# Performance work log

Measured on AMD Instinct MI355X. Metric: run time of the kernel, lower is better.

The kernel has to match this reference:

```python
import jax, jax.numpy as jnp
import numpy as np

TEMPERATURE = 0.08
NEG = -9e15  # matches torch masked_fill value
EPS = 1e-8   # F.cosine_similarity eps


def setup_inputs() -> dict:
    key = jax.random.key(0)
    inputs = jax.random.normal(key, (8192, 512), dtype=jnp.float32)
    return {"inputs": inputs}


def reference(inputs):
    N = inputs.shape[0]
    # cosine similarity via normalize + GEMM (avoids NxNxD broadcast)
    norms = jnp.maximum(jnp.linalg.norm(inputs, axis=-1, keepdims=True), EPS)
    z = inputs / norms
    sim = z @ z.T  # [N, N]
    # mask self-similarity BEFORE temperature scaling (as in the torch code)
    diag = jnp.eye(N, dtype=bool)
    sim = jnp.where(diag, NEG, sim)
    sim = sim / TEMPERATURE
    # positive of row i is column (i - N//2) % N (eye rolled by N//2 along dim 0)
    idx = jnp.arange(N)
    pos_idx = (idx - N // 2) % N
    pos = jnp.take_along_axis(sim, pos_idx[:, None], axis=1)[:, 0]  # [N]
    nll = jnp.mean(-pos + jax.scipy.special.logsumexp(sim, axis=-1))
    # rank of the positive: counting-based equivalent of
    # cat([pos, sim_masked]).argsort(desc).argmin() with stable ties
    masked = sim.at[idx, pos_idx].set(NEG)
    positive_ranking = jnp.sum(masked > pos[:, None], axis=-1)  # [N] int
    return positive_ranking, nll
```

## Files before the change

kernel.cpp:

```cpp
#include <hip/hip_runtime.h>
#include <cstdint>
#include <cstddef>

#define NROW 8192
#define DIM  512
#define HALF 4096
#define INV_T 12.5f
#define LDSW 64

typedef __bf16 bf16x8  __attribute__((ext_vector_type(8)));
typedef float  floatx4 __attribute__((ext_vector_type(4)));

__device__ __forceinline__ float bf2f_lo(unsigned u) { return __uint_as_float(u << 16); }
__device__ __forceinline__ float bf2f_hi(unsigned u) { return __uint_as_float(u & 0xffff0000u); }
__device__ __forceinline__ unsigned short f2bf(float f) {
    unsigned u = __float_as_uint(f);
    u += 0x7fffu + ((u >> 16) & 1u);
    return (unsigned short)(u >> 16);
}

__global__ void knorm(const float* __restrict__ x, unsigned short* __restrict__ z,
                      float* __restrict__ sumexp, float* __restrict__ cnt,
                      float* __restrict__ nll_acc) {
    int id = blockIdx.x * 256 + threadIdx.x;
    if (id < NROW) { sumexp[id] = 0.f; cnt[id] = 0.f; }
    if (id == 0) nll_acc[0] = 0.f;

    int row  = blockIdx.x * 4 + (threadIdx.x >> 6);
    int lane = threadIdx.x & 63;
    const float* xr = x + (size_t)row * DIM + lane * 8;
    float4 v0 = ((const float4*)xr)[0];
    float4 v1 = ((const float4*)xr)[1];
    float ss = v0.x*v0.x + v0.y*v0.y + v0.z*v0.z + v0.w*v0.w
             + v1.x*v1.x + v1.y*v1.y + v1.z*v1.z + v1.w*v1.w;
    #pragma unroll
    for (int m = 1; m < 64; m <<= 1) ss += __shfl_xor(ss, m);
    float inv = 1.0f / fmaxf(sqrtf(ss), 1e-8f);
    uint4 o;
    o.x = (unsigned)f2bf(v0.x * inv) | ((unsigned)f2bf(v0.y * inv) << 16);
    o.y = (unsigned)f2bf(v0.z * inv) | ((unsigned)f2bf(v0.w * inv) << 16);
    o.z = (unsigned)f2bf(v1.x * inv) | ((unsigned)f2bf(v1.y * inv) << 16);
    o.w = (unsigned)f2bf(v1.z * inv) | ((unsigned)f2bf(v1.w * inv) << 16);
    int sl = (lane & 56) | ((lane & 7) ^ (row & 7));
    *(uint4*)(z + (size_t)row * DIM + sl * 8) = o;
}

__global__ void kpos(const unsigned short* __restrict__ z, float* __restrict__ pos) {
    int row  = blockIdx.x * 4 + (threadIdx.x >> 6);
    int lane = threadIdx.x & 63;
    int prow = (row + HALF) & (NROW - 1);
    uint4 a = *(const uint4*)(z + (size_t)row  * DIM + lane * 8);
    uint4 b = *(const uint4*)(z + (size_t)prow * DIM + lane * 8);
    float s = bf2f_lo(a.x)*bf2f_lo(b.x) + bf2f_hi(a.x)*bf2f_hi(b.x)
            + bf2f_lo(a.y)*bf2f_lo(b.y) + bf2f_hi(a.y)*bf2f_hi(b.y)
            + bf2f_lo(a.z)*bf2f_lo(b.z) + bf2f_hi(a.z)*bf2f_hi(b.z)
            + bf2f_lo(a.w)*bf2f_lo(b.w) + bf2f_hi(a.w)*bf2f_hi(b.w);
    #pragma unroll
    for (int m = 1; m < 64; m <<= 1) s += __shfl_xor(s, m);
    if (lane == 0) pos[row] = s;
}

__global__ __launch_bounds__(256) void kgemm(const unsigned short* __restrict__ z,
                                             const float* __restrict__ pos,
                                             float* __restrict__ sumexp,
                                             float* __restrict__ cnt) {
    __shared__ __align__(16) unsigned short As[128 * LDSW];
    __shared__ __align__(16) unsigned short Bs[128 * LDSW];
    __shared__ float pos_r[128];
    __shared__ float pos_c[128];

    const int b = blockIdx.x;
    int bi = (int)((129.0f - sqrtf((float)(16641 - 8 * b))) * 0.5f);
    while (bi * (129 - bi) / 2 > b) --bi;
    while ((bi + 1) * (128 - bi) / 2 <= b) ++bi;
    const int bj = bi + (b - bi * (129 - bi) / 2);
    const int r0 = bi * 128;
    const int c0 = bj * 128;
    const bool offdiag = (bi != bj);

    const int t = threadIdx.x;
    const int w = t >> 6, lane = t & 63;
    const int wm = w >> 1, wn = w & 1;

    if (t < 128) pos_r[t] = pos[r0 + t];
    else         pos_c[t - 128] = pos[c0 + (t - 128)];

    floatx4 acc[4][4];
    #pragma unroll
    for (int i = 0; i < 4; ++i)
        #pragma unroll
        for (int j = 0; j < 4; ++j)
            acc[i][j] = floatx4{0.f, 0.f, 0.f, 0.f};

    const int lrow8 = lane >> 3;
    const int lcol  = (lane & 7) * 8;

    for (int kk = 0; kk < 8; ++kk) {
        const int k0 = kk * 64;
        #pragma unroll
        for (int it = 0; it < 4; ++it) {
            const int c = it * 4 + w;
            const unsigned short* gA = z + (size_t)(r0 + c * 8 + lrow8) * DIM + k0 + lcol;
            const unsigned short* gB = z + (size_t)(c0 + c * 8 + lrow8) * DIM + k0 + lcol;
            __builtin_amdgcn_global_load_lds(
                (const __attribute__((address_space(1))) unsigned int*)gA,
                (__attribute__((address_space(3))) unsigned int*)(As + c * 512),
                16, 0, 0);
            __builtin_amdgcn_global_load_lds(
                (const __attribute__((address_space(1))) unsigned int*)gB,
                (__attribute__((address_space(3))) unsigned int*)(Bs + c * 512),
                16, 0, 0);
        }
        __syncthreads();
        const int q = lane >> 4, cid16 = lane & 15;
        #pragma unroll
        for (int ks = 0; ks < 2; ++ks) {
            bf16x8 af[4], bfv[4];
            #pragma unroll
            for (int f = 0; f < 4; ++f) {
                const int ar = wm * 64 + f * 16 + cid16;
                const int br = wn * 64 + f * 16 + cid16;
                const int pa = (4 * ks + q) ^ (ar & 7);
                const int pb = (4 * ks + q) ^ (br & 7);
                af[f]  = *(const bf16x8*)(As + ar * LDSW + pa * 8);
                bfv[f] = *(const bf16x8*)(Bs + br * LDSW + pb * 8);
            }
            #pragma unroll
            for (int fm = 0; fm < 4; ++fm)
                #pragma unroll
                for (int fn = 0; fn < 4; ++fn)
                    acc[fm][fn] = __builtin_amdgcn_mfma_f32_16x16x32_bf16(
                        af[fm], bfv[fn], acc[fm][fn], 0, 0, 0);
        }
        __syncthreads();
    }

    const int rgrp = lane >> 4;
    const int cid  = lane & 15;

    #pragma unroll
    for (int fm = 0; fm < 4; ++fm) {
        #pragma unroll
        for (int r = 0; r < 4; ++r) {
            const int li = wm * 64 + fm * 16 + rgrp * 4 + r;
            const int i  = r0 + li;
            const float pv = pos_r[li];
            const int pj = (i + HALF) & (NROW - 1);
            float esum = 0.f, csum = 0.f;
            #pragma unroll
            for (int fn = 0; fn < 4; ++fn) {
                const int j = c0 + wn * 64 + fn * 16 + cid;
                const float s = acc[fm][fn][r];
                const bool diag = (j == i);
                esum += diag ? 0.f : __expf(s * INV_T - INV_T);
                csum += (!diag && (j != pj) && (s > pv)) ? 1.f : 0.f;
            }
            #pragma unroll
            for (int m = 1; m < 16; m <<= 1) {
                esum += __shfl_xor(esum, m);
                csum += __shfl_xor(csum, m);
            }
            if (cid == 0) {
                atomicAdd(&sumexp[i], esum);
                atomicAdd(&cnt[i], csum);
            }
        }
    }

    if (offdiag) {
        #pragma unroll
        for (int fn = 0; fn < 4; ++fn) {
            const int lj = wn * 64 + fn * 16 + cid;
            const int j  = c0 + lj;
            const float pvc = pos_c[lj];
            const int pjc = (j + HALF) & (NROW - 1);
            float ec = 0.f, cc = 0.f;
            #pragma unroll
            for (int fm = 0; fm < 4; ++fm) {
                #pragma unroll
                for (int r = 0; r < 4; ++r) {
                    const int i = r0 + wm * 64 + fm * 16 + rgrp * 4 + r;
                    const float s = acc[fm][fn][r];
                    ec += __expf(s * INV_T - INV_T);
                    cc += ((i != pjc) && (s > pvc)) ? 1.f : 0.f;
                }
            }
            ec += __shfl_xor(ec, 16); ec += __shfl_xor(ec, 32);
            cc += __shfl_xor(cc, 16); cc += __shfl_xor(cc, 32);
            if (rgrp == 0) {
                atomicAdd(&sumexp[j], ec);
                atomicAdd(&cnt[j], cc);
            }
        }
    }
}

__global__ void NCELoss_3126736191777_kernel(const float* __restrict__ cnt,
                                             const float* __restrict__ sumexp,
                                             const float* __restrict__ pos,
                                             float* __restrict__ out,
                                             float* __restrict__ nll_acc) {
    __shared__ float red[4];
    const int t = threadIdx.x;
    const int r = blockIdx.x * 256 + t;
    float c = cnt[r], se = sumexp[r], p = pos[r];
    float v;
    if (p != p || fabsf(p) > 1.05f) v = 60000.0f;
    else if (se == 0.0f)            v = 40000.0f;
    else if (c < 0.0f)              v = 25000.0f;
    else                            v = c;
    out[r] = v;
    float local = -p * INV_T + INV_T + __logf(se);
    #pragma unroll
    for (int m = 1; m < 64; m <<= 1) local += __shfl_xor(local, m);
    if ((t & 63) == 0) red[t >> 6] = local;
    __syncthreads();
    if (t == 0) atomicAdd(nll_acc, red[0] + red[1] + red[2] + red[3]);
}

__global__ void klast(const float* __restrict__ nll_acc, float* __restrict__ out) {
    out[NROW] = nll_acc[0] / (float)NROW;
}

extern "C" void kernel_launch(void* const* d_in, const int* in_sizes, int n_in,
                              void* d_out, int out_size, void* d_ws, size_t ws_size,
                              hipStream_t stream) {
    (void)in_sizes; (void)n_in; (void)out_size; (void)ws_size;
    const float* x = (const float*)d_in[0];

    char* base = (char*)d_ws;
    float* pos     = (float*)(base);
    float* sumexp  = (float*)(base + (size_t)NROW * 4);
    float* cnt     = (float*)(base + (size_t)NROW * 8);
    float* nll_acc = (float*)(base + (size_t)NROW * 12);
    unsigned short* z = (unsigned short*)(base + (size_t)NROW * 12 + 4096);
    float* out = (float*)d_out;

    knorm<<<NROW / 4, 256, 0, stream>>>(x, z, sumexp, cnt, nll_acc);
    kpos<<<NROW / 4, 256, 0, stream>>>(z, pos);
    kgemm<<<2080, 256, 0, stream>>>(z, pos, sumexp, cnt);
    NCELoss_3126736191777_kernel<<<NROW / 256, 256, 0, stream>>>(cnt, sumexp, pos, out, nll_acc);
    klast<<<1, 64, 0, stream>>>(nll_acc, out);
}
```

Measured before the change: 191.1 us.

## Fuse final mean into reduction kernel, relax atomics, raise occupancy hint

Removes the separate single-thread final kernel by having the last block, found with an atomic ticket counter, write the mean NLL. Replaces atomicAdd with relaxed agent-scope atomics. Adds a min-blocks-per-CU launch bound of 5 to the GEMM kernel and drops the LDS staging of positive similarities in favour of direct global loads in the epilogue. The launch-bound hint may force register limits or spills, and the direct pos loads add global traffic in the epilogue.

```diff
diff --git a/kernel.cpp b/kernel.cpp
--- a/kernel.cpp
+++ b/kernel.cpp
@@ -19,12 +19,16 @@
     return (unsigned short)(u >> 16);
 }
 
+__device__ __forceinline__ void atom_addf(float* p, float v) {
+    __hip_atomic_fetch_add(p, v, __ATOMIC_RELAXED, __HIP_MEMORY_SCOPE_AGENT);
+}
+
 __global__ void knorm(const float* __restrict__ x, unsigned short* __restrict__ z,
                       float* __restrict__ sumexp, float* __restrict__ cnt,
-                      float* __restrict__ nll_acc) {
+                      float* __restrict__ nll_acc, int* __restrict__ done) {
     int id = blockIdx.x * 256 + threadIdx.x;
     if (id < NROW) { sumexp[id] = 0.f; cnt[id] = 0.f; }
-    if (id == 0) nll_acc[0] = 0.f;
+    if (id == 0) { nll_acc[0] = 0.f; done[0] = 0; }
 
     int row  = blockIdx.x * 4 + (threadIdx.x >> 6);
     int lane = threadIdx.x & 63;
@@ -60,14 +64,12 @@
     if (lane == 0) pos[row] = s;
 }
 
-__global__ __launch_bounds__(256) void kgemm(const unsigned short* __restrict__ z,
-                                             const float* __restrict__ pos,
-                                             float* __restrict__ sumexp,
-                                             float* __restrict__ cnt) {
+__global__ __launch_bounds__(256, 5) void kgemm(const unsigned short* __restrict__ z,
+                                                const float* __restrict__ pos,
+                                                float* __restrict__ sumexp,
+                                                float* __restrict__ cnt) {
     __shared__ __align__(16) unsigned short As[128 * LDSW];
     __shared__ __align__(16) unsigned short Bs[128 * LDSW];
-    __shared__ float pos_r[128];
-    __shared__ float pos_c[128];
 
     const int b = blockIdx.x;
     int bi = (int)((129.0f - sqrtf((float)(16641 - 8 * b))) * 0.5f);
@@ -81,9 +83,6 @@
     const int t = threadIdx.x;
     const int w = t >> 6, lane = t & 63;
     const int wm = w >> 1, wn = w & 1;
-
-    if (t < 128) pos_r[t] = pos[r0 + t];
-    else         pos_c[t - 128] = pos[c0 + (t - 128)];
 
     floatx4 acc[4][4];
     #pragma unroll
@@ -144,7 +143,7 @@
         for (int r = 0; r < 4; ++r) {
             const int li = wm * 64 + fm * 16 + rgrp * 4 + r;
             const int i  = r0 + li;
-            const float pv = pos_r[li];
+            const float pv = pos[i];
             const int pj = (i + HALF) & (NROW - 1);
             float esum = 0.f, csum = 0.f;
             #pragma unroll
@@ -161,8 +160,8 @@
                 csum += __shfl_xor(csum, m);
             }
             if (cid == 0) {
-                atomicAdd(&sumexp[i], esum);
-                atomicAdd(&cnt[i], csum);
+                atom_addf(&sumexp[i], esum);
+                atom_addf(&cnt[i], csum);
             }
         }
     }
@@ -172,7 +171,7 @@
         for (int fn = 0; fn < 4; ++fn) {
             const int lj = wn * 64 + fn * 16 + cid;
             const int j  = c0 + lj;
-            const float pvc = pos_c[lj];
+            const float pvc = pos[j];
             const int pjc = (j + HALF) & (NROW - 1);
             float ec = 0.f, cc = 0.f;
             #pragma unroll
@@ -188,8 +187,8 @@
             ec += __shfl_xor(ec, 16); ec += __shfl_xor(ec, 32);
             cc += __shfl_xor(cc, 16); cc += __shfl_xor(cc, 32);
             if (rgrp == 0) {
-                atomicAdd(&sumexp[j], ec);
-                atomicAdd(&cnt[j], cc);
+                atom_addf(&sumexp[j], ec);
+                atom_addf(&cnt[j], cc);
             }
         }
     }
@@ -199,7 +198,8 @@
                                              const float* __restrict__ sumexp,
                                              const float* __restrict__ pos,
                                              float* __restrict__ out,
-                                             float* __restrict__ nll_acc) {
+                                             float* __restrict__ nll_acc,
+                                             int* __restrict__ done) {
     __shared__ float red[4];
     const int t = threadIdx.x;
     const int r = blockIdx.x * 256 + t;
@@ -215,11 +215,16 @@
     for (int m = 1; m < 64; m <<= 1) local += __shfl_xor(local, m);
     if ((t & 63) == 0) red[t >> 6] = local;
     __syncthreads();
-    if (t == 0) atomicAdd(nll_acc, red[0] + red[1] + red[2] + red[3]);
-}
-
-__global__ void klast(const float* __restrict__ nll_acc, float* __restrict__ out) {
-    out[NROW] = nll_acc[0] / (float)NROW;
+    if (t == 0) {
+        atom_addf(nll_acc, red[0] + red[1] + red[2] + red[3]);
+        __threadfence();
+        int ticket = __hip_atomic_fetch_add(done, 1, __ATOMIC_ACQ_REL,
+                                            __HIP_MEMORY_SCOPE_AGENT);
+        if (ticket == (int)gridDim.x - 1) {
+            __threadfence();
+            out[NROW] = nll_acc[0] / (float)NROW;
+        }
+    }
 }
 
 extern "C" void kernel_launch(void* const* d_in, const int* in_sizes, int n_in,
@@ -233,12 +238,12 @@
     float* sumexp  = (float*)(base + (size_t)NROW * 4);
     float* cnt     = (float*)(base + (size_t)NROW * 8);
     float* nll_acc = (float*)(base + (size_t)NROW * 12);
+    int*   done    = (int*)(base + (size_t)NROW * 12 + 64);
     unsigned short* z = (unsigned short*)(base + (size_t)NROW * 12 + 4096);
     float* out = (float*)d_out;
 
-    knorm<<<NROW / 4, 256, 0, stream>>>(x, z, sumexp, cnt, nll_acc);
+    knorm<<<NROW / 4, 256, 0, stream>>>(x, z, sumexp, cnt, nll_acc, done);
     kpos<<<NROW / 4, 256, 0, stream>>>(z, pos);
     kgemm<<<2080, 256, 0, stream>>>(z, pos, sumexp, cnt);
-    NCELoss_3126736191777_kernel<<<NROW / 256, 256, 0, stream>>>(cnt, sumexp, pos, out, nll_acc);
-    klast<<<1, 64, 0, stream>>>(nll_acc, out);
-}
+    NCELoss_3126736191777_kernel<<<NROW / 256, 256, 0, stream>>>(cnt, sumexp, pos, out, nll_acc, done);
+}
```

New measurement: 252.4 us. 1.32x slower.
